# Optimization experiments

Hardware: AMD Instinct MI355X
Metric: run time of the kernel (lower is better)

## Reference

```python
import jax, jax.numpy as jnp
import numpy as np


def _conv2d(x, w):
    # x: [B,Cin,H,W], w: [Cout,Cin,kh,kw], stride 1, SAME padding
    return jax.lax.conv_general_dilated(x, w, (1, 1), 'SAME',
                                        dimension_numbers=('NCHW', 'OIHW', 'NCHW'))


def _conv1d(x, w):
    # x: [B,Cin,L], w: [Cout,Cin,k], stride 1, SAME padding
    return jax.lax.conv_general_dilated(x, w, (1,), 'SAME',
                                        dimension_numbers=('NCH', 'OIH', 'NCH'))


def setup_inputs() -> dict:
    key = jax.random.key(0)
    ks = jax.random.split(key, 5)
    B, cin, cout, H, W = 8, 256, 256, 64, 64
    x = jax.random.normal(ks[0], (B, cin, H, W), dtype=jnp.float32)
    # Conv weights, small init ~ 1/sqrt(fan_in)
    w_qkv = jax.random.normal(ks[1], (3 * cout, cin, 3, 3), dtype=jnp.float32) * (1.0 / np.sqrt(cin * 9))
    w_mod = jax.random.normal(ks[2], (2 * cout, cout, 3), dtype=jnp.float32) * (1.0 / np.sqrt(cout * 3))
    w_res = jax.random.normal(ks[3], (cout, cin, 1, 1), dtype=jnp.float32) * (1.0 / np.sqrt(cin))
    w_gate = jax.random.normal(ks[4], (cout, cin + cout, 1, 1), dtype=jnp.float32) * (1.0 / np.sqrt(cin + cout))
    return {'x': x, 'w_qkv': w_qkv, 'w_mod': w_mod, 'w_res': w_res, 'w_gate': w_gate}


def reference(x, w_qkv, w_mod, w_res, w_gate):
    B, C, H, W = x.shape
    cout = w_res.shape[0]
    L = H * W
    # qkv projection, then split and flatten spatial dims
    qkv = _conv2d(x, w_qkv).reshape(B, 3, cout, L)  # [B,3,cout,L]
    q, k, v = qkv[:, 0], qkv[:, 1], qkv[:, 2]       # each [B,cout,L]
    # modulation from v along the spatial axis (Conv1d)
    mod = _conv1d(v, w_mod).reshape(B, 2, cout, L)
    qm, km = mod[:, 0], mod[:, 1]
    # negate-relu softmax modulated scores over spatial axis
    m_q = jax.nn.softmax(-jax.nn.relu(q * qm), axis=-1)  # [B,cout,L]
    m_k = jax.nn.softmax(-jax.nn.relu(k * km), axis=-1)  # [B,cout,L]
    scale = 1.0 / jnp.sqrt(jnp.asarray(C, dtype=x.dtype))
    m_attn = jax.nn.softmax(jnp.einsum('bcl,bdl->bcd', m_q, m_k) * scale, axis=-1)  # [B,cout,cout]
    y = jnp.einsum('bcd,bdl->bcl', m_attn, v).reshape(B, cout, H, W)
    # sigmoid-gated residual blend
    g = jax.nn.sigmoid(_conv2d(jnp.concatenate([y, x], axis=1), w_gate))
    return g * _conv2d(x, w_res) + (1.0 - g) * y
```

## Files before the change

kernel.cpp:

```cpp
#include <hip/hip_runtime.h>
#include <cstdint>

typedef unsigned short u16;
using bf16x8 = __attribute__((ext_vector_type(8))) short;
using f32x4  = __attribute__((ext_vector_type(4))) float;

struct alignas(16) V16 { uint32_t a, b, c, d; };
struct alignas(8)  U16x4 { u16 a, b, c, d; };
struct alignas(16) F4 { float x, y, z, w; };

__device__ __forceinline__ u16 f2bf(float f) {
  uint32_t u = __float_as_uint(f);
  u += 0x7fffu + ((u >> 16) & 1u);
  return (u16)(u >> 16);
}
__device__ __forceinline__ float bf2f(u16 h) {
  return __uint_as_float(((uint32_t)h) << 16);
}

#define GLOAD16(g, l) __builtin_amdgcn_global_load_lds(                         \
    (const __attribute__((address_space(1))) uint32_t*)(g),                     \
    (__attribute__((address_space(3))) uint32_t*)(l), 16, 0, 0)

template<int MODE, int MF, int FUSE = 0>
__global__ __launch_bounds__(512, 2) void gemmOv_bf16(
    const u16* __restrict__ A, const u16* __restrict__ B, u16* __restrict__ otr,
    int sA, int sB, int64_t bBatch, int trStride, int64_t trBatch, int MT,
    const u16* __restrict__ zpage,
    const u16* __restrict__ fq = nullptr, u16* __restrict__ eOut = nullptr,
    float* __restrict__ partS = nullptr)
{
  constexpr int NS = (MODE == 2) ? 36 : 12;
  constexpr int ASL = MF * 2048;
  constexpr int SLAB = ASL + 16384;
  __shared__ __align__(16) u16 lds[2 * SLAB];

  const int tid = threadIdx.x;
  const int q = gridDim.x >> 3;
  const int flat = (blockIdx.x & 7) * q + (blockIdx.x >> 3);
  const int per_b = MT * 16;
  const int b = flat / per_b, rem = flat % per_b;
  const int ntile = rem / MT, mtile = rem % MT;
  const int m0 = mtile * (MF * 32), n0 = ntile * 256;
  const u16* Bb = B + (int64_t)b * bBatch;

  const int lane = tid & 63, wave = tid >> 6;
  const int wm = wave >> 2, wn = wave & 3;
  const int lr = lane & 15, lc = lane >> 4;

  const int lrow8 = lane >> 3;
  const int sch  = lane & 7;
  const int scs  = sch ^ (lrow8 & 7);
  const u16* aSrc[MF / 2];
  const u16* bSrc[4];
  int bRow[4];
#pragma unroll
  for (int j = 0; j < MF / 2; ++j)
    aSrc[j] = A + (int64_t)(m0 + wave * (MF * 4) + j * 8 + lrow8) * sA + scs * 8;
#pragma unroll
  for (int j = 0; j < 4; ++j) {
    bRow[j] = n0 + wave * 32 + j * 8 + lrow8;
    bSrc[j] = Bb + (int64_t)bRow[j] * sB + scs * 8;
  }

  auto stageA = [&](int s) {
    const int kOff = (s >> 2) * 256 + ((s & 3) << 6);
    u16* dst = lds + (s & 1) * SLAB + wave * (MF / 2) * 512;
#pragma unroll
    for (int j = 0; j < MF / 2; ++j)
      GLOAD16(aSrc[j] + kOff, dst + j * 512);
  };
  auto stageB = [&](int s) {
    const int tap = s >> 2, kc = (s & 3) << 6;
    int off, dh = 0, dw = 0;
    if constexpr (MODE == 2) { dh = tap / 3 - 1; dw = tap % 3 - 1; off = dh * 64 + dw; }
    else                     { off = tap - 1; }
    u16* dst = lds + (s & 1) * SLAB + ASL + wave * 2048;
#pragma unroll
    for (int j = 0; j < 4; ++j) {
      bool ok;
      if constexpr (MODE == 2) {
        int hh = (bRow[j] >> 6) + dh, ww = (bRow[j] & 63) + dw;
        ok = ((unsigned)hh < 64u) && ((unsigned)ww < 64u);
      } else {
        ok = ((unsigned)(bRow[j] + off) < 4096u);
      }
      const u16* src = ok ? (bSrc[j] + (int64_t)off * sB + kc) : zpage;
      GLOAD16(src, dst + j * 512);
    }
  };

  f32x4 acc[MF][4];
#pragma unroll
  for (int i = 0; i < MF; ++i)
#pragma unroll
    for (int j = 0; j < 4; ++j) acc[i][j] = f32x4{0.f, 0.f, 0.f, 0.f};

  stageA(0); stageB(0);
  asm volatile("s_waitcnt vmcnt(0)" ::: "memory");
  __builtin_amdgcn_s_barrier();
  __builtin_amdgcn_sched_barrier(0);

  for (int s = 0; s < NS; ++s) {
    const u16* As = lds + (s & 1) * SLAB;
    const u16* Bs = As + ASL;
    const bool pf = (s + 1 < NS);
    bf16x8 bfr[4], af[MF];

#pragma unroll
    for (int nf = 0; nf < 4; ++nf) {
      int row = wn * 64 + nf * 16 + lr;
      bfr[nf] = *(const bf16x8*)&Bs[row * 64 + ((lc ^ (row & 7)) * 8)];
    }
#pragma unroll
    for (int mf = 0; mf < MF; ++mf) {
      int row = wm * (MF * 16) + mf * 16 + lr;
      af[mf] = *(const bf16x8*)&As[row * 64 + ((lc ^ (row & 7)) * 8)];
    }
    if (pf) stageA(s + 1);
#pragma unroll
    for (int mf = 0; mf < MF; ++mf)
#pragma unroll
      for (int nf = 0; nf < 4; ++nf)
        acc[mf][nf] = __builtin_amdgcn_mfma_f32_16x16x32_bf16(af[mf], bfr[nf], acc[mf][nf], 0, 0, 0);

#pragma unroll
    for (int nf = 0; nf < 4; ++nf) {
      int row = wn * 64 + nf * 16 + lr;
      bfr[nf] = *(const bf16x8*)&Bs[row * 64 + (((4 + lc) ^ (row & 7)) * 8)];
    }
#pragma unroll
    for (int mf = 0; mf < MF; ++mf) {
      int row = wm * (MF * 16) + mf * 16 + lr;
      af[mf] = *(const bf16x8*)&As[row * 64 + (((4 + lc) ^ (row & 7)) * 8)];
    }
    if (pf) stageB(s + 1);
#pragma unroll
    for (int mf = 0; mf < MF; ++mf)
#pragma unroll
      for (int nf = 0; nf < 4; ++nf)
        acc[mf][nf] = __builtin_amdgcn_mfma_f32_16x16x32_bf16(af[mf], bfr[nf], acc[mf][nf], 0, 0, 0);

    if (pf) {
      asm volatile("s_waitcnt vmcnt(0)" ::: "memory");
      __builtin_amdgcn_s_barrier();
      __builtin_amdgcn_sched_barrier(0);
    }
  }

  if constexpr (FUSE) {
    const u16* qk = fq + (int64_t)b * 4096 * 768;
    u16* eb = eOut + (int64_t)b * 512 * 4096;
    float* ps = partS + (int64_t)b * 512 * 64;
#pragma unroll
    for (int mf = 0; mf < MF; ++mf) {
      const int mbase = m0 + wm * (MF * 16) + mf * 16 + lc * 4;
      float sp[4] = {0.f, 0.f, 0.f, 0.f};
#pragma unroll
      for (int nf = 0; nf < 4; ++nf) {
        int n = n0 + wn * 64 + nf * 16 + lr;
        U16x4 qv = *(const U16x4*)(qk + (int64_t)n * 768 + mbase);
        const u16* qp = (const u16*)&qv;
        f32x4 v = acc[mf][nf];
#pragma unroll
        for (int r = 0; r < 4; ++r) {
          float z = bf2f(qp[r]) * v[r];
          float e = __expf(z > 0.f ? -z : 0.f);
          sp[r] += e;
          eb[(int64_t)(mbase + r) * 4096 + n] = f2bf(e);
        }
      }
#pragma unroll
      for (int r = 0; r < 4; ++r) {
        float sv = sp[r];
        sv += __shfl_xor(sv, 1);
        sv += __shfl_xor(sv, 2);
        sv += __shfl_xor(sv, 4);
        sv += __shfl_xor(sv, 8);
        if (lr == 0)
          ps[(int64_t)(mbase + r) * 64 + ntile * 4 + wn] = sv;
      }
    }
  } else {
#pragma unroll
    for (int mf = 0; mf < MF; ++mf)
#pragma unroll
      for (int nf = 0; nf < 4; ++nf) {
        f32x4 v = acc[mf][nf];
        int m = m0 + wm * (MF * 16) + mf * 16 + lc * 4;
        int n = n0 + wn * 64 + nf * 16 + lr;
        U16x4 pk{f2bf(v[0]), f2bf(v[1]), f2bf(v[2]), f2bf(v[3])};
        *(U16x4*)(otr + trBatch * b + (int64_t)n * trStride + m) = pk;
      }
  }
}

template<int MODE, bool WR_RM, bool WR_TR, bool WR_FOUT = false, bool DUAL = false>
__global__ __launch_bounds__(256) void gemm_bf16(
    const u16* __restrict__ A, const u16* __restrict__ B,
    float* __restrict__ orm, u16* __restrict__ otr,
    int Kc, int sA, int64_t aBatch,
    int sB, int64_t bBatch,
    int rmStride, int64_t rmBatch,
    int trStride, int64_t trBatch,
    int nsplit, int kStep, int64_t splitOut,
    const u16* __restrict__ zpage,
    const u16* __restrict__ fyt, const u16* __restrict__ A2)
{
  constexpr int NTAPS = (MODE == 2) ? 9 : (MODE == 1 ? 3 : 1);
  __shared__ __align__(16) u16 As[128 * 32];
  __shared__ __align__(16) u16 Bs[128 * 32];
  __shared__ __align__(16) u16 As2[128 * 32];

  const int tid = threadIdx.x;
  int b = blockIdx.z, split = 0;
  if (nsplit > 1) { split = b % nsplit; b /= nsplit; }
  const int m0  = blockIdx.y * 128;
  const int n0  = blockIdx.x * 128;
  const int lane = tid & 63, wave = tid >> 6;
  const int wm = wave >> 1, wn = wave & 1;
  const int lr = lane & 15, lc = lane >> 4;

  f32x4 acc[4][4];
#pragma unroll
  for (int i = 0; i < 4; ++i)
#pragma unroll
    for (int j = 0; j < 4; ++j) acc[i][j] = f32x4{0.f, 0.f, 0.f, 0.f};
  f32x4 acc2[4][4];
  if constexpr (DUAL) {
#pragma unroll
    for (int i = 0; i < 4; ++i)
#pragma unroll
      for (int j = 0; j < 4; ++j) acc2[i][j] = f32x4{0.f, 0.f, 0.f, 0.f};
  }

  const u16* Ab = A + (int64_t)b * aBatch + split * kStep;
  const u16* Bb = B + (int64_t)b * bBatch + split * kStep;

  const int srow = tid >> 2;
  const int sc   = tid & 3;
  const int scs  = sc ^ (srow & 3);

  for (int t = 0; t < NTAPS; ++t) {
    int dh = 0, dw = 0, off = 0;
    if constexpr (MODE == 2) { dh = t / 3 - 1; dw = t % 3 - 1; off = dh * 64 + dw; }
    if constexpr (MODE == 1) { off = t - 1; }

    for (int kc = 0; kc < Kc; kc += 32) {
      const int kA = t * Kc + kc;
      const bool dualK = DUAL && (kA >= 256);
#pragma unroll
      for (int it = 0; it < 2; ++it) {
        int row = srow + it * 64;
        GLOAD16(Ab + (int64_t)(m0 + row) * sA + kA + scs * 8,
                &As[wave * 512 + it * 2048]);
      }
      if constexpr (DUAL) {
        if (dualK) {
#pragma unroll
          for (int it = 0; it < 2; ++it) {
            int row = srow + it * 64;
            GLOAD16(A2 + (int64_t)(m0 + row) * 256 + (kA - 256) + scs * 8,
                    &As2[wave * 512 + it * 2048]);
          }
        }
      }
#pragma unroll
      for (int it = 0; it < 2; ++it) {
        int row = srow + it * 64;
        int l = n0 + row;
        int gl = l + off;
        bool ok = true;
        if constexpr (MODE == 2) {
          int hh = (l >> 6) + dh, ww = (l & 63) + dw;
          ok = ((unsigned)hh < 64u) && ((unsigned)ww < 64u);
        }
        if constexpr (MODE == 1) { ok = ((unsigned)gl < 4096u); }
        const u16* src = ok ? (Bb + (int64_t)gl * sB + kc + scs * 8) : zpage;
        GLOAD16(src, &Bs[wave * 512 + it * 2048]);
      }
      __syncthreads();

      bf16x8 af[4], bfr[4];
#pragma unroll
      for (int mf = 0; mf < 4; ++mf) {
        int row = wm * 64 + mf * 16 + lr;
        int cs = lc ^ (row & 3);
        af[mf] = *(const bf16x8*)&As[row * 32 + cs * 8];
      }
#pragma unroll
      for (int nf = 0; nf < 4; ++nf) {
        int row = wn * 64 + nf * 16 + lr;
        int cs = lc ^ (row & 3);
        bfr[nf] = *(const bf16x8*)&Bs[row * 32 + cs * 8];
      }
#pragma unroll
      for (int mf = 0; mf < 4; ++mf)
#pragma unroll
        for (int nf = 0; nf < 4; ++nf)
          acc[mf][nf] = __builtin_amdgcn_mfma_f32_16x16x32_bf16(af[mf], bfr[nf], acc[mf][nf], 0, 0, 0);
      if constexpr (DUAL) {
        if (dualK) {
          bf16x8 af2[4];
#pragma unroll
          for (int mf = 0; mf < 4; ++mf) {
            int row = wm * 64 + mf * 16 + lr;
            int cs = lc ^ (row & 3);
            af2[mf] = *(const bf16x8*)&As2[row * 32 + cs * 8];
          }
#pragma unroll
          for (int mf = 0; mf < 4; ++mf)
#pragma unroll
            for (int nf = 0; nf < 4; ++nf)
              acc2[mf][nf] = __builtin_amdgcn_mfma_f32_16x16x32_bf16(af2[mf], bfr[nf], acc2[mf][nf], 0, 0, 0);
        }
      }
      __syncthreads();
    }
  }

#pragma unroll
  for (int mf = 0; mf < 4; ++mf) {
#pragma unroll
    for (int nf = 0; nf < 4; ++nf) {
      f32x4 v = acc[mf][nf];
      int m = m0 + wm * 64 + mf * 16 + lc * 4;
      int n = n0 + wn * 64 + nf * 16 + lr;
      if constexpr (WR_FOUT) {
        int64_t off = rmBatch * b + (int64_t)m * rmStride + n;
        float* p = orm + off;
        f32x4 rv = acc2[mf][nf];
        U16x4 yv = *(const U16x4*)(fyt + ((int64_t)(b * 4096 + n)) * 512 + m);
        const u16* yp = (const u16*)&yv;
#pragma unroll
        for (int r = 0; r < 4; ++r) {
          float g = 1.f / (1.f + __expf(-v[r]));
          p[(int64_t)r * rmStride] = g * rv[r] + (1.f - g) * bf2f(yp[r]);
        }
      }
      if constexpr (WR_RM) {
        float* p = orm + splitOut * split + rmBatch * b + (int64_t)m * rmStride + n;
#pragma unroll
        for (int r = 0; r < 4; ++r) p[(int64_t)r * rmStride] = v[r];
      }
      if constexpr (WR_TR) {
        U16x4 pk{f2bf(v[0]), f2bf(v[1]), f2bf(v[2]), f2bf(v[3])};
        *(U16x4*)(otr + trBatch * b + (int64_t)n * trStride + m) = pk;
      }
    }
  }
}

__global__ void k_prep(const float* __restrict__ wqkv, const float* __restrict__ wmod,
                       const float* __restrict__ wgate, const float* __restrict__ wres,
                       u16* __restrict__ Wa, u16* __restrict__ Wb,
                       u16* __restrict__ Wg, u16* __restrict__ Wr,
                       uint32_t* __restrict__ zpage) {
  int bid = blockIdx.x, t = threadIdx.x;
  if (bid < 6912) {
    int idx = bid * 256 + t;
    if (idx < 768 * 2304) {
      int oc = idx / 2304, r = idx % 2304;
      int tap = r >> 8, ic = r & 255;
      Wa[idx] = f2bf(wqkv[((oc * 256 + ic) * 3 + tap / 3) * 3 + tap % 3]);
    }
  } else if (bid < 8448) {
    int idx = (bid - 6912) * 256 + t;
    if (idx < 512 * 768) {
      int oc = idx / 768, r = idx % 768;
      int tap = r >> 8, ic = r & 255;
      Wb[idx] = f2bf(wmod[(oc * 256 + ic) * 3 + tap]);
    }
  } else if (bid < 8960) {
    int idx = (bid - 8448) * 256 + t;
    if (idx < 131072) Wg[idx] = f2bf(wgate[idx]);
  } else if (bid < 9216) {
    int idx = (bid - 8960) * 256 + t;
    if (idx < 65536) Wr[idx] = f2bf(wres[idx]);
  } else {
    if (t < 64) zpage[t] = 0u;
  }
}

__global__ __launch_bounds__(256) void k_xT(const float* __restrict__ x, u16* __restrict__ ycat) {
  __shared__ float tile[64 * 68];
  int b = blockIdx.z, c0 = blockIdx.y * 64, l0 = blockIdx.x * 64;
  int t = threadIdx.x;
  int cc = t >> 2, part = t & 3;
  const float* xp = x + ((int64_t)(b * 256 + c0 + cc)) * 4096 + l0 + part * 16;
#pragma unroll
  for (int j = 0; j < 4; ++j) {
    F4 v = *(const F4*)(xp + j * 4);
    float* tp = &tile[cc * 68 + part * 16 + j * 4];
    tp[0] = v.x; tp[1] = v.y; tp[2] = v.z; tp[3] = v.w;
  }
  __syncthreads();
  int l = t >> 2;
  u16* op = ycat + ((int64_t)b * 4096 + l0 + l) * 512 + 256 + c0 + part * 16;
  __align__(16) u16 tmp[16];
#pragma unroll
  for (int j = 0; j < 16; ++j) tmp[j] = f2bf(tile[(part * 16 + j) * 68 + l]);
  *(V16*)(op) = *(V16*)&tmp[0];
  *(V16*)(op + 8) = *(V16*)&tmp[8];
}

__global__ void k_statsB64(const float* __restrict__ part, float* __restrict__ inv) {
  int idx = blockIdx.x * 256 + threadIdx.x;
  float S = 0.f;
#pragma unroll
  for (int s = 0; s < 64; ++s) S += part[(int64_t)idx * 64 + s];
  inv[idx] = 1.0f / S;
}

__global__ __launch_bounds__(256) void k_softmax_attn(
    const float* __restrict__ sc, const float* __restrict__ invS,
    u16* __restrict__ ma, int nsplit, int64_t splitOff) {
  int c = blockIdx.x, b = blockIdx.y;
  int64_t base = ((int64_t)b * 256 + c) * 256;
  int t = threadIdx.x;
  float z = 0.f;
  for (int s = 0; s < nsplit; ++s) z += sc[(int64_t)s * splitOff + base + t];
  float iq = invS[(int64_t)b * 512 + c];
  float ik = invS[(int64_t)b * 512 + 256 + t];
  z *= iq * ik * 0.0625f;
  __shared__ float red[256];
  red[t] = z; __syncthreads();
  for (int s = 128; s > 0; s >>= 1) { if (t < s) red[t] = fmaxf(red[t], red[t + s]); __syncthreads(); }
  float M = red[0]; __syncthreads();
  float p = __expf(z - M);
  red[t] = p; __syncthreads();
  for (int s = 128; s > 0; s >>= 1) { if (t < s) red[t] += red[t + s]; __syncthreads(); }
  ma[base + t] = f2bf(p / red[0]);
}

extern "C" void kernel_launch(void* const* d_in, const int* in_sizes, int n_in,
                              void* d_out, int out_size, void* d_ws, size_t ws_size,
                              hipStream_t stream) {
  (void)in_sizes; (void)n_in; (void)out_size; (void)ws_size;
  const float* x      = (const float*)d_in[0];
  const float* w_qkv  = (const float*)d_in[1];
  const float* w_mod  = (const float*)d_in[2];
  const float* w_res  = (const float*)d_in[3];
  const float* w_gate = (const float*)d_in[4];
  float* out = (float*)d_out;

  char* p = (char*)d_ws;
  auto take = [&](size_t n) { void* r = (void*)p; p += (n + 255) & ~(size_t)255; return r; };
  u16*    zpage  = (u16*)take(256);
  u16*    qkvT   = (u16*)take(50331648);
  u16*    ycatT  = (u16*)take(33554432);
  u16*    eT     = (u16*)take(33554432);
  float*  scores = (float*)take(16777216);
  u16*    mattn  = (u16*)take(1048576);
  float*  partS  = (float*)take(1048576);
  float*  invS   = (float*)take(16384);
  u16*    Wa     = (u16*)take(3538944);
  u16*    Wb     = (u16*)take(786432);
  u16*    Wg     = (u16*)take(262144);
  u16*    Wr     = (u16*)take(131072);

  k_prep<<<9217, 256, 0, stream>>>(w_qkv, w_mod, w_gate, w_res,
                                   Wa, Wb, Wg, Wr, (uint32_t*)zpage);
  k_xT<<<dim3(64, 4, 8), 256, 0, stream>>>(x, ycatT);

  gemmOv_bf16<2, 6><<<512, 512, 0, stream>>>(
      Wa, ycatT + 256, qkvT,
      2304, 512, (int64_t)4096 * 512,
      768, (int64_t)4096 * 768, 4, zpage);

  gemmOv_bf16<1, 8, 1><<<256, 512, 0, stream>>>(
      Wb, qkvT + 512, nullptr,
      768, 768, (int64_t)4096 * 768,
      0, 0, 2, zpage,
      qkvT, eT, partS);

  k_statsB64<<<16, 256, 0, stream>>>(partS, invS);

  gemm_bf16<0, true, false><<<dim3(2, 2, 64), 256, 0, stream>>>(
      eT, eT + (int64_t)256 * 4096, scores, nullptr,
      512, 4096, (int64_t)512 * 4096,
      4096, (int64_t)512 * 4096,
      256, (int64_t)256 * 256,
      0, 0,
      8, 512, (int64_t)8 * 256 * 256, zpage, nullptr, nullptr);

  k_softmax_attn<<<dim3(256, 8), 256, 0, stream>>>(
      scores, invS, mattn, 8, (int64_t)8 * 256 * 256);

  gemm_bf16<0, false, true><<<dim3(32, 2, 8), 256, 0, stream>>>(
      mattn, qkvT + 512, nullptr, ycatT,
      256, 256, (int64_t)256 * 256,
      768, (int64_t)4096 * 768,
      0, 0,
      512, (int64_t)4096 * 512,
      1, 0, 0, zpage, nullptr, nullptr);

  gemm_bf16<0, false, false, true, true><<<dim3(32, 2, 8), 256, 0, stream>>>(
      Wg, ycatT, out, nullptr,
      512, 512, 0,
      512, (int64_t)4096 * 512,
      4096, (int64_t)256 * 4096,
      0, 0,
      1, 0, 0, zpage, ycatT, Wr);
}
```

Baseline: 248.2 us.

## Fuse attention-apply GEMM and gated blend into one tail kernel via LDS

Replaces the two final GEMM launches (m_attn·v writing y to global, then the gate/residual GEMM reading it back) with a single 512-thread kernel. Each block computes all 256 output channels of y for a 128-position tile and keeps y in shared memory, then runs the gate and residual GEMMs directly from it. This removes the global write and re-read of y and one launch. In exchange it uses about 100KB of LDS per block, which limits occupancy, and the grid shrinks to 256 blocks. The scores GEMM is also specialized into its own simpler kernel.

```diff
diff --git a/kernel.cpp b/kernel.cpp
--- a/kernel.cpp
+++ b/kernel.cpp
@@ -195,22 +195,15 @@
   }
 }
 
-template<int MODE, bool WR_RM, bool WR_TR, bool WR_FOUT = false, bool DUAL = false>
-__global__ __launch_bounds__(256) void gemm_bf16(
+__global__ __launch_bounds__(256) void gemm_scores(
     const u16* __restrict__ A, const u16* __restrict__ B,
-    float* __restrict__ orm, u16* __restrict__ otr,
-    int Kc, int sA, int64_t aBatch,
-    int sB, int64_t bBatch,
+    float* __restrict__ orm,
+    int sA, int64_t aBatch, int sB, int64_t bBatch,
     int rmStride, int64_t rmBatch,
-    int trStride, int64_t trBatch,
-    int nsplit, int kStep, int64_t splitOut,
-    const u16* __restrict__ zpage,
-    const u16* __restrict__ fyt, const u16* __restrict__ A2)
+    int nsplit, int kStep, int64_t splitOut)
 {
-  constexpr int NTAPS = (MODE == 2) ? 9 : (MODE == 1 ? 3 : 1);
   __shared__ __align__(16) u16 As[128 * 32];
   __shared__ __align__(16) u16 Bs[128 * 32];
-  __shared__ __align__(16) u16 As2[128 * 32];
 
   const int tid = threadIdx.x;
   int b = blockIdx.z, split = 0;
@@ -226,13 +219,6 @@
   for (int i = 0; i < 4; ++i)
 #pragma unroll
     for (int j = 0; j < 4; ++j) acc[i][j] = f32x4{0.f, 0.f, 0.f, 0.f};
-  f32x4 acc2[4][4];
-  if constexpr (DUAL) {
-#pragma unroll
-    for (int i = 0; i < 4; ++i)
-#pragma unroll
-      for (int j = 0; j < 4; ++j) acc2[i][j] = f32x4{0.f, 0.f, 0.f, 0.f};
-  }
 
   const u16* Ab = A + (int64_t)b * aBatch + split * kStep;
   const u16* Bb = B + (int64_t)b * bBatch + split * kStep;
@@ -241,114 +227,195 @@
   const int sc   = tid & 3;
   const int scs  = sc ^ (srow & 3);
 
-  for (int t = 0; t < NTAPS; ++t) {
-    int dh = 0, dw = 0, off = 0;
-    if constexpr (MODE == 2) { dh = t / 3 - 1; dw = t % 3 - 1; off = dh * 64 + dw; }
-    if constexpr (MODE == 1) { off = t - 1; }
-
-    for (int kc = 0; kc < Kc; kc += 32) {
-      const int kA = t * Kc + kc;
-      const bool dualK = DUAL && (kA >= 256);
-#pragma unroll
-      for (int it = 0; it < 2; ++it) {
-        int row = srow + it * 64;
-        GLOAD16(Ab + (int64_t)(m0 + row) * sA + kA + scs * 8,
-                &As[wave * 512 + it * 2048]);
-      }
-      if constexpr (DUAL) {
-        if (dualK) {
-#pragma unroll
-          for (int it = 0; it < 2; ++it) {
-            int row = srow + it * 64;
-            GLOAD16(A2 + (int64_t)(m0 + row) * 256 + (kA - 256) + scs * 8,
-                    &As2[wave * 512 + it * 2048]);
-          }
-        }
-      }
-#pragma unroll
-      for (int it = 0; it < 2; ++it) {
-        int row = srow + it * 64;
-        int l = n0 + row;
-        int gl = l + off;
-        bool ok = true;
-        if constexpr (MODE == 2) {
-          int hh = (l >> 6) + dh, ww = (l & 63) + dw;
-          ok = ((unsigned)hh < 64u) && ((unsigned)ww < 64u);
-        }
-        if constexpr (MODE == 1) { ok = ((unsigned)gl < 4096u); }
-        const u16* src = ok ? (Bb + (int64_t)gl * sB + kc + scs * 8) : zpage;
-        GLOAD16(src, &Bs[wave * 512 + it * 2048]);
-      }
-      __syncthreads();
-
-      bf16x8 af[4], bfr[4];
-#pragma unroll
-      for (int mf = 0; mf < 4; ++mf) {
-        int row = wm * 64 + mf * 16 + lr;
-        int cs = lc ^ (row & 3);
-        af[mf] = *(const bf16x8*)&As[row * 32 + cs * 8];
-      }
-#pragma unroll
-      for (int nf = 0; nf < 4; ++nf) {
-        int row = wn * 64 + nf * 16 + lr;
-        int cs = lc ^ (row & 3);
-        bfr[nf] = *(const bf16x8*)&Bs[row * 32 + cs * 8];
-      }
-#pragma unroll
-      for (int mf = 0; mf < 4; ++mf)
-#pragma unroll
-        for (int nf = 0; nf < 4; ++nf)
-          acc[mf][nf] = __builtin_amdgcn_mfma_f32_16x16x32_bf16(af[mf], bfr[nf], acc[mf][nf], 0, 0, 0);
-      if constexpr (DUAL) {
-        if (dualK) {
-          bf16x8 af2[4];
-#pragma unroll
-          for (int mf = 0; mf < 4; ++mf) {
-            int row = wm * 64 + mf * 16 + lr;
-            int cs = lc ^ (row & 3);
-            af2[mf] = *(const bf16x8*)&As2[row * 32 + cs * 8];
-          }
-#pragma unroll
-          for (int mf = 0; mf < 4; ++mf)
-#pragma unroll
-            for (int nf = 0; nf < 4; ++nf)
-              acc2[mf][nf] = __builtin_amdgcn_mfma_f32_16x16x32_bf16(af2[mf], bfr[nf], acc2[mf][nf], 0, 0, 0);
-        }
-      }
-      __syncthreads();
-    }
-  }
-
-#pragma unroll
-  for (int mf = 0; mf < 4; ++mf) {
+  for (int kc = 0; kc < 512; kc += 32) {
+#pragma unroll
+    for (int it = 0; it < 2; ++it) {
+      int row = srow + it * 64;
+      GLOAD16(Ab + (int64_t)(m0 + row) * sA + kc + scs * 8,
+              &As[wave * 512 + it * 2048]);
+      GLOAD16(Bb + (int64_t)(n0 + row) * sB + kc + scs * 8,
+              &Bs[wave * 512 + it * 2048]);
+    }
+    __syncthreads();
+
+    bf16x8 af[4], bfr[4];
+#pragma unroll
+    for (int mf = 0; mf < 4; ++mf) {
+      int row = wm * 64 + mf * 16 + lr;
+      af[mf] = *(const bf16x8*)&As[row * 32 + ((lc ^ (row & 3)) * 8)];
+    }
+#pragma unroll
+    for (int nf = 0; nf < 4; ++nf) {
+      int row = wn * 64 + nf * 16 + lr;
+      bfr[nf] = *(const bf16x8*)&Bs[row * 32 + ((lc ^ (row & 3)) * 8)];
+    }
+#pragma unroll
+    for (int mf = 0; mf < 4; ++mf)
+#pragma unroll
+      for (int nf = 0; nf < 4; ++nf)
+        acc[mf][nf] = __builtin_amdgcn_mfma_f32_16x16x32_bf16(af[mf], bfr[nf], acc[mf][nf], 0, 0, 0);
+    __syncthreads();
+  }
+
+#pragma unroll
+  for (int mf = 0; mf < 4; ++mf)
 #pragma unroll
     for (int nf = 0; nf < 4; ++nf) {
       f32x4 v = acc[mf][nf];
       int m = m0 + wm * 64 + mf * 16 + lc * 4;
       int n = n0 + wn * 64 + nf * 16 + lr;
-      if constexpr (WR_FOUT) {
-        int64_t off = rmBatch * b + (int64_t)m * rmStride + n;
-        float* p = orm + off;
-        f32x4 rv = acc2[mf][nf];
-        U16x4 yv = *(const U16x4*)(fyt + ((int64_t)(b * 4096 + n)) * 512 + m);
-        const u16* yp = (const u16*)&yv;
-#pragma unroll
-        for (int r = 0; r < 4; ++r) {
-          float g = 1.f / (1.f + __expf(-v[r]));
-          p[(int64_t)r * rmStride] = g * rv[r] + (1.f - g) * bf2f(yp[r]);
-        }
-      }
-      if constexpr (WR_RM) {
-        float* p = orm + splitOut * split + rmBatch * b + (int64_t)m * rmStride + n;
-#pragma unroll
-        for (int r = 0; r < 4; ++r) p[(int64_t)r * rmStride] = v[r];
-      }
-      if constexpr (WR_TR) {
-        U16x4 pk{f2bf(v[0]), f2bf(v[1]), f2bf(v[2]), f2bf(v[3])};
-        *(U16x4*)(otr + trBatch * b + (int64_t)n * trStride + m) = pk;
-      }
-    }
-  }
+      float* p = orm + splitOut * split + rmBatch * b + (int64_t)m * rmStride + n;
+#pragma unroll
+      for (int r = 0; r < 4; ++r) p[(int64_t)r * rmStride] = v[r];
+    }
+}
+
+__global__ __launch_bounds__(512) void k_tail(
+    const u16* __restrict__ mattn, const u16* __restrict__ qkvT,
+    const u16* __restrict__ ycatT, const u16* __restrict__ Wg,
+    const u16* __restrict__ Wr, float* __restrict__ out)
+{
+  __shared__ __align__(16) u16 As[256 * 32];
+  __shared__ __align__(16) u16 As2[256 * 32];
+  __shared__ __align__(16) u16 Bs[128 * 32];
+  __shared__ __align__(16) u16 yT[128 * 260];
+
+  const int b = blockIdx.y, l0 = blockIdx.x * 128;
+  const int tid = threadIdx.x;
+  const int lane = tid & 63, wave = tid >> 6;
+  const int wm = wave >> 1, wn = wave & 1;
+  const int lr = lane & 15, lc = lane >> 4;
+
+  const int srow = tid >> 2, sc = tid & 3;
+  const int scs = sc ^ (srow & 3);
+
+  f32x4 acc[4][4];
+#pragma unroll
+  for (int i = 0; i < 4; ++i)
+#pragma unroll
+    for (int j = 0; j < 4; ++j) acc[i][j] = f32x4{0.f, 0.f, 0.f, 0.f};
+
+  const u16* Am = mattn + (int64_t)b * 65536;
+  const u16* Vv = qkvT + (int64_t)b * 4096 * 768 + 512;
+  for (int kc = 0; kc < 256; kc += 32) {
+#pragma unroll
+    for (int it = 0; it < 2; ++it) {
+      int row = srow + it * 128;
+      GLOAD16(Am + (int64_t)row * 256 + kc + scs * 8,
+              &As[wave * 512 + it * 4096]);
+    }
+    GLOAD16(Vv + (int64_t)(l0 + srow) * 768 + kc + scs * 8, &Bs[wave * 512]);
+    __syncthreads();
+
+    bf16x8 af[4], bfr[4];
+#pragma unroll
+    for (int mf = 0; mf < 4; ++mf) {
+      int row = wm * 64 + mf * 16 + lr;
+      af[mf] = *(const bf16x8*)&As[row * 32 + ((lc ^ (row & 3)) * 8)];
+    }
+#pragma unroll
+    for (int nf = 0; nf < 4; ++nf) {
+      int row = wn * 64 + nf * 16 + lr;
+      bfr[nf] = *(const bf16x8*)&Bs[row * 32 + ((lc ^ (row & 3)) * 8)];
+    }
+#pragma unroll
+    for (int mf = 0; mf < 4; ++mf)
+#pragma unroll
+      for (int nf = 0; nf < 4; ++nf)
+        acc[mf][nf] = __builtin_amdgcn_mfma_f32_16x16x32_bf16(af[mf], bfr[nf], acc[mf][nf], 0, 0, 0);
+    __syncthreads();
+  }
+
+#pragma unroll
+  for (int mf = 0; mf < 4; ++mf)
+#pragma unroll
+    for (int nf = 0; nf < 4; ++nf) {
+      f32x4 v = acc[mf][nf];
+      int m = wm * 64 + mf * 16 + lc * 4;
+      int n = wn * 64 + nf * 16 + lr;
+      U16x4 pk{f2bf(v[0]), f2bf(v[1]), f2bf(v[2]), f2bf(v[3])};
+      *(U16x4*)&yT[n * 260 + m] = pk;
+    }
+  __syncthreads();
+
+  f32x4 acc2[4][4];
+#pragma unroll
+  for (int i = 0; i < 4; ++i)
+#pragma unroll
+    for (int j = 0; j < 4; ++j) {
+      acc[i][j] = f32x4{0.f, 0.f, 0.f, 0.f};
+      acc2[i][j] = f32x4{0.f, 0.f, 0.f, 0.f};
+    }
+
+  const u16* Xc = ycatT + (int64_t)b * 4096 * 512;
+  for (int kc = 0; kc < 512; kc += 32) {
+    const bool xk = (kc >= 256);
+#pragma unroll
+    for (int it = 0; it < 2; ++it) {
+      int row = srow + it * 128;
+      GLOAD16(Wg + (int64_t)row * 512 + kc + scs * 8,
+              &As[wave * 512 + it * 4096]);
+    }
+    if (xk) {
+#pragma unroll
+      for (int it = 0; it < 2; ++it) {
+        int row = srow + it * 128;
+        GLOAD16(Wr + (int64_t)row * 256 + (kc - 256) + scs * 8,
+                &As2[wave * 512 + it * 4096]);
+      }
+      GLOAD16(Xc + (int64_t)(l0 + srow) * 512 + kc + scs * 8, &Bs[wave * 512]);
+    }
+    __syncthreads();
+
+    bf16x8 af[4], bfr[4];
+#pragma unroll
+    for (int nf = 0; nf < 4; ++nf) {
+      int row = wn * 64 + nf * 16 + lr;
+      if (xk) bfr[nf] = *(const bf16x8*)&Bs[row * 32 + ((lc ^ (row & 3)) * 8)];
+      else    bfr[nf] = *(const bf16x8*)&yT[row * 260 + kc + lc * 8];
+    }
+#pragma unroll
+    for (int mf = 0; mf < 4; ++mf) {
+      int row = wm * 64 + mf * 16 + lr;
+      af[mf] = *(const bf16x8*)&As[row * 32 + ((lc ^ (row & 3)) * 8)];
+    }
+#pragma unroll
+    for (int mf = 0; mf < 4; ++mf)
+#pragma unroll
+      for (int nf = 0; nf < 4; ++nf)
+        acc[mf][nf] = __builtin_amdgcn_mfma_f32_16x16x32_bf16(af[mf], bfr[nf], acc[mf][nf], 0, 0, 0);
+    if (xk) {
+      bf16x8 af2[4];
+#pragma unroll
+      for (int mf = 0; mf < 4; ++mf) {
+        int row = wm * 64 + mf * 16 + lr;
+        af2[mf] = *(const bf16x8*)&As2[row * 32 + ((lc ^ (row & 3)) * 8)];
+      }
+#pragma unroll
+      for (int mf = 0; mf < 4; ++mf)
+#pragma unroll
+        for (int nf = 0; nf < 4; ++nf)
+          acc2[mf][nf] = __builtin_amdgcn_mfma_f32_16x16x32_bf16(af2[mf], bfr[nf], acc2[mf][nf], 0, 0, 0);
+    }
+    __syncthreads();
+  }
+
+#pragma unroll
+  for (int mf = 0; mf < 4; ++mf)
+#pragma unroll
+    for (int nf = 0; nf < 4; ++nf) {
+      f32x4 g4 = acc[mf][nf], r4 = acc2[mf][nf];
+      int m = wm * 64 + mf * 16 + lc * 4;
+      int n = wn * 64 + nf * 16 + lr;
+      U16x4 yv = *(const U16x4*)&yT[n * 260 + m];
+      const u16* yp = (const u16*)&yv;
+      float* p = out + (int64_t)b * 256 * 4096 + (int64_t)m * 4096 + l0 + n;
+#pragma unroll
+      for (int r = 0; r < 4; ++r) {
+        float g = 1.f / (1.f + __expf(-g4[r]));
+        p[(int64_t)r * 4096] = g * r4[r] + (1.f - g) * bf2f(yp[r]);
+      }
+    }
 }
 
 __global__ void k_prep(const float* __restrict__ wqkv, const float* __restrict__ wmod,
@@ -476,30 +543,15 @@
 
   k_statsB64<<<16, 256, 0, stream>>>(partS, invS);
 
-  gemm_bf16<0, true, false><<<dim3(2, 2, 64), 256, 0, stream>>>(
-      eT, eT + (int64_t)256 * 4096, scores, nullptr,
-      512, 4096, (int64_t)512 * 4096,
+  gemm_scores<<<dim3(2, 2, 64), 256, 0, stream>>>(
+      eT, eT + (int64_t)256 * 4096, scores,
+      4096, (int64_t)512 * 4096,
       4096, (int64_t)512 * 4096,
       256, (int64_t)256 * 256,
-      0, 0,
-      8, 512, (int64_t)8 * 256 * 256, zpage, nullptr, nullptr);
+      8, 512, (int64_t)8 * 256 * 256);
 
   k_softmax_attn<<<dim3(256, 8), 256, 0, stream>>>(
       scores, invS, mattn, 8, (int64_t)8 * 256 * 256);
 
-  gemm_bf16<0, false, true><<<dim3(32, 2, 8), 256, 0, stream>>>(
-      mattn, qkvT + 512, nullptr, ycatT,
-      256, 256, (int64_t)256 * 256,
-      768, (int64_t)4096 * 768,
-      0, 0,
-      512, (int64_t)4096 * 512,
-      1, 0, 0, zpage, nullptr, nullptr);
-
-  gemm_bf16<0, false, false, true, true><<<dim3(32, 2, 8), 256, 0, stream>>>(
-      Wg, ycatT, out, nullptr,
-      512, 512, 0,
-      512, (int64_t)4096 * 512,
-      4096, (int64_t)256 * 4096,
-      0, 0,
-      1, 0, 0, zpage, ycatT, Wr);
-}
+  k_tail<<<dim3(32, 8), 512, 0, stream>>>(mattn, qkvT, ycatT, Wg, Wr, out);
+}
```

After: 225.7 us. 9.1% less time.
